# Kernel optimization log

Hardware: AMD Instinct MI355X
Metric: run time of the kernel (lower is better)

## Reference

```python
import jax, jax.numpy as jnp
import numpy as np

B, C, CI, H, W = 8, 256, 128, 64, 64
EPS = 1e-5


def conv1x1(x, w, b):
    # x: [B,C,H,W], w: [O,C], b: [O] -> [B,O,H,W]
    return jnp.einsum('bchw,oc->bohw', x, w) + b[None, :, None, None]


def maxpool2(x):
    # 2x2 max pool, stride 2 (NCHW)
    b, c, h, w = x.shape
    return x.reshape(b, c, h // 2, 2, w // 2, 2).max(axis=(3, 5))


def setup_inputs() -> dict:
    key = jax.random.key(0)
    ks = jax.random.split(key, 14)
    s_in = 1.0 / np.sqrt(C)
    s_ci = 1.0 / np.sqrt(CI)
    return {
        'x': jax.random.normal(ks[0], (B, C, H, W), jnp.float32),
        'w_theta': jax.random.normal(ks[1], (CI, C), jnp.float32) * s_in,
        'b_theta': jax.random.normal(ks[2], (CI,), jnp.float32) * 0.01,
        'w_phi': jax.random.normal(ks[3], (CI, C), jnp.float32) * s_in,
        'b_phi': jax.random.normal(ks[4], (CI,), jnp.float32) * 0.01,
        'w_g': jax.random.normal(ks[5], (CI, C), jnp.float32) * s_in,
        'b_g': jax.random.normal(ks[6], (CI,), jnp.float32) * 0.01,
        'w_w': jax.random.normal(ks[7], (C, CI), jnp.float32) * s_ci,
        'b_w': jax.random.normal(ks[8], (C,), jnp.float32) * 0.01,
        'bn_gamma': jax.random.normal(ks[9], (C,), jnp.float32) * 0.1,
        'bn_beta': jax.random.normal(ks[10], (C,), jnp.float32) * 0.1,
        'bn_mean': jax.random.normal(ks[11], (C,), jnp.float32) * 0.1,
        'bn_var': jax.random.uniform(ks[12], (C,), jnp.float32) + 0.5,
    }


def reference(x, w_theta, b_theta, w_phi, b_phi, w_g, b_g,
              w_w, b_w, bn_gamma, bn_beta, bn_mean, bn_var):
    b = x.shape[0]
    theta_x = conv1x1(x, w_theta, b_theta).reshape(b, CI, -1)            # [B,Ci,N]
    phi_x = maxpool2(conv1x1(x, w_phi, b_phi)).reshape(b, CI, -1)        # [B,Ci,M]
    g_x = maxpool2(conv1x1(x, w_g, b_g)).reshape(b, CI, -1)              # [B,Ci,M]
    m = phi_x.shape[-1]
    # unnormalized attention: f = theta^T phi / M  -> [B,N,M]
    f = jnp.einsum('bcn,bcm->bnm', theta_x, phi_x) / m
    y = jnp.einsum('bnm,bcm->bcn', f, g_x).reshape(b, CI, H, W)          # [B,Ci,H,W]
    w_y = conv1x1(y, w_w, b_w)                                           # [B,C,H,W]
    inv = jax.lax.rsqrt(bn_var + EPS)
    bn = (w_y - bn_mean[None, :, None, None]) * (bn_gamma * inv)[None, :, None, None] \
         + bn_beta[None, :, None, None]
    return bn + x
```

## Files before the change

kernel.cpp:

```cpp
#include <hip/hip_runtime.h>


typedef __attribute__((ext_vector_type(8))) short bf16x8;
typedef __attribute__((ext_vector_type(4))) float f32x4;
typedef unsigned short u16;
typedef unsigned int u32;

constexpr int Cc = 256, NnC = 4096;
constexpr float kEps = 1e-5f;

__device__ __forceinline__ u16 f2b(float f) {
  u32 u = __float_as_uint(f);
  return (u16)((u + 0x7fffu + ((u >> 16) & 1u)) >> 16);
}
__device__ __forceinline__ float b2f(u16 h) {
  return __uint_as_float(((u32)h) << 16);
}
__device__ __forceinline__ u32 pack2(float a, float b) {
  return (u32)f2b(a) | ((u32)f2b(b) << 16);
}
__device__ __forceinline__ void gl16(const void* g, void* l) {
  __builtin_amdgcn_global_load_lds(
      (const __attribute__((address_space(1))) void*)g,
      (__attribute__((address_space(3))) void*)l, 16, 0, 0);
}

__global__ __launch_bounds__(256) void prepw_kernel(
    const float* __restrict__ wp, const float* __restrict__ wg,
    u16* __restrict__ Wfg) {
  const int idx = blockIdx.x * 256 + threadIdx.x;
  const int r = idx >> 8, c = idx & 255;
  Wfg[idx] = f2b(r < 128 ? wp[r * 256 + c] : wg[(r - 128) * 256 + c]);
}

__global__ __launch_bounds__(256) void prepx_kernel(const float* __restrict__ x,
                                                    u16* __restrict__ xT) {
  __shared__ float sm[64][65];
  const int b = blockIdx.z, c0 = blockIdx.y * 64, n0 = blockIdx.x * 64;
  const int tid = threadIdx.x;
  {
    const int n = tid & 63, cg = tid >> 6;
#pragma unroll
    for (int i = 0; i < 16; ++i) {
      const int c = cg * 16 + i;
      sm[c][n] = x[((size_t)(b * Cc + c0 + c)) * NnC + n0 + n];
    }
  }
  __syncthreads();
  {
    const int n = tid >> 2, q = tid & 3;
    u16 v[16];
#pragma unroll
    for (int j = 0; j < 16; ++j) v[j] = f2b(sm[q * 16 + j][n]);
    uint4 o0, o1;
    o0.x = v[0] | ((u32)v[1] << 16);
    o0.y = v[2] | ((u32)v[3] << 16);
    o0.z = v[4] | ((u32)v[5] << 16);
    o0.w = v[6] | ((u32)v[7] << 16);
    o1.x = v[8] | ((u32)v[9] << 16);
    o1.y = v[10] | ((u32)v[11] << 16);
    o1.z = v[12] | ((u32)v[13] << 16);
    o1.w = v[14] | ((u32)v[15] << 16);
    uint4* dst = (uint4*)(xT + ((size_t)(b * NnC + n0 + n)) * Cc + c0 + q * 16);
    dst[0] = o0;
    dst[1] = o1;
  }
}

__global__ __launch_bounds__(256) void convfg_kernel(
    const u16* __restrict__ xT, const u16* __restrict__ Wfg,
    const float* __restrict__ b_phi, const float* __restrict__ b_g,
    u16* __restrict__ phiT, u16* __restrict__ gT) {
  __shared__ u16 sm[2][2][8192];
  const int mt = blockIdx.x, nt = blockIdx.y, b = blockIdx.z;
  const int n0 = nt * 128;
  const int tid = threadIdx.x;
  const int w = tid >> 6, lane = tid & 63;
  const int r16 = lane & 15, kg = lane >> 4;
  const int oh = (w & 1) * 64, nh = (w >> 1) * 64;

  auto stage = [&](int buf, int k0) {
#pragma unroll
    for (int i = 0; i < 4; ++i) {
      const int lin = i * 4096 + tid * 16;
      const int row = lin >> 7, byte = lin & 127;
      gl16((const char*)Wfg + (size_t)(mt * 128 + row) * 512 + k0 * 2 +
               (byte ^ ((row & 7) << 4)),
           (char*)&sm[buf][0][0] + lin);
    }
#pragma unroll
    for (int i = 0; i < 4; ++i) {
      const int lin = i * 4096 + tid * 16;
      const int row = lin >> 7, byte = lin & 127;
      gl16((const char*)xT + ((size_t)(b * NnC + n0 + row) * Cc + k0) * 2 +
               (byte ^ ((row & 7) << 4)),
           (char*)&sm[buf][1][0] + lin);
    }
  };

  f32x4 acc[4][4];
#pragma unroll
  for (int i = 0; i < 4; ++i)
#pragma unroll
    for (int j = 0; j < 4; ++j) acc[i][j] = (f32x4)0.f;

  stage(0, 0);
  __syncthreads();
  for (int kt = 0; kt < 4; ++kt) {
    if (kt < 3) stage((kt + 1) & 1, (kt + 1) * 64);
    const char* A = (const char*)&sm[kt & 1][0][0];
    const char* Bm = (const char*)&sm[kt & 1][1][0];
#pragma unroll
    for (int ks = 0; ks < 2; ++ks) {
      bf16x8 af[4], bfr[4];
#pragma unroll
      for (int f = 0; f < 4; ++f) {
        const int o = oh + f * 16 + r16;
        af[f] = *(const bf16x8*)(A + ((o * 128 + ks * 64 + kg * 16) ^
                                      ((o & 7) << 4)));
        const int n = nh + f * 16 + r16;
        bfr[f] = *(const bf16x8*)(Bm + ((n * 128 + ks * 64 + kg * 16) ^
                                        ((n & 7) << 4)));
      }
#pragma unroll
      for (int fo = 0; fo < 4; ++fo)
#pragma unroll
        for (int fn = 0; fn < 4; ++fn)
          acc[fo][fn] = __builtin_amdgcn_mfma_f32_16x16x32_bf16(
              af[fo], bfr[fn], acc[fo][fn], 0, 0, 0);
    }
    __syncthreads();
  }

  const float* bias = (mt == 0) ? b_phi : b_g;
  u16* ldst = (u16*)&sm[0][0][0];
#pragma unroll
  for (int fo = 0; fo < 4; ++fo) {
    const int obase = oh + fo * 16 + kg * 4;
    const float b0 = bias[obase], b1 = bias[obase + 1], b2 = bias[obase + 2],
                b3 = bias[obase + 3];
#pragma unroll
    for (int fn = 0; fn < 4; ++fn) {
      const int n = nh + fn * 16 + r16;
      const f32x4 v = acc[fo][fn];
      uint2 p;
      p.x = pack2(v.x + b0, v.y + b1);
      p.y = pack2(v.z + b2, v.w + b3);
      *(uint2*)((char*)ldst + ((n * 256 + obase * 2) ^ ((n & 7) << 4))) = p;
    }
  }
  __syncthreads();

  u16* dst = (mt == 0) ? phiT : gT;
  const int ci = tid >> 1, half = tid & 1;
#pragma unroll
  for (int i = 0; i < 16; ++i) {
    const int mw = half * 16 + i;
    const int n00 = 2 * mw;
    float v0 = b2f(*(const u16*)((const char*)ldst +
                                 ((n00 * 256 + ci * 2) ^ ((n00 & 7) << 4))));
    float v1 = b2f(*(const u16*)((const char*)ldst +
                                 (((n00 + 1) * 256 + ci * 2) ^ (((n00 + 1) & 7) << 4))));
    float v2 = b2f(*(const u16*)((const char*)ldst +
                                 (((n00 + 64) * 256 + ci * 2) ^ (((n00 + 64) & 7) << 4))));
    float v3 = b2f(*(const u16*)((const char*)ldst +
                                 (((n00 + 65) * 256 + ci * 2) ^ (((n00 + 65) & 7) << 4))));
    const float mx = fmaxf(fmaxf(v0, v1), fmaxf(v2, v3));
    dst[((size_t)(b * 128 + ci)) * 1024 + nt * 32 + mw] = f2b(mx);
  }
}

__global__ __launch_bounds__(256) void g2_kernel(const u16* __restrict__ phiT,
                                                 const u16* __restrict__ gT,
                                                 float* __restrict__ A_g2) {
  __shared__ u16 sm[2][12288];
  const int ch0 = blockIdx.x * 64, b = blockIdx.y;
  const int tid = threadIdx.x;
  const int w = tid >> 6, lane = tid & 63;
  const int r16 = lane & 15, kg = lane >> 4;
  const int cih = (w & 1) * 64, cch = (w >> 1) * 32;

  auto stage = [&](int buf, int m0) {
#pragma unroll
    for (int i = 0; i < 4; ++i) {
      const int lin = i * 4096 + tid * 16;
      const int row = lin >> 7, byte = lin & 127;
      gl16((const char*)gT + ((size_t)(b * 128 + row) * 1024 + m0) * 2 +
               (byte ^ ((row & 7) << 4)),
           (char*)&sm[buf][0] + lin);
    }
#pragma unroll
    for (int i = 0; i < 2; ++i) {
      const int lin = i * 4096 + tid * 16;
      const int row = lin >> 7, byte = lin & 127;
      gl16((const char*)phiT + ((size_t)(b * 128 + ch0 + row) * 1024 + m0) * 2 +
               (byte ^ ((row & 7) << 4)),
           (char*)&sm[buf][8192] + lin);
    }
  };

  f32x4 acc[4][2];
#pragma unroll
  for (int i = 0; i < 4; ++i)
#pragma unroll
    for (int j = 0; j < 2; ++j) acc[i][j] = (f32x4)0.f;

  stage(0, 0);
  __syncthreads();
  for (int kt = 0; kt < 16; ++kt) {
    if (kt < 15) stage((kt + 1) & 1, (kt + 1) * 64);
    const char* A = (const char*)&sm[kt & 1][0];
    const char* Bp = A + 16384;
#pragma unroll
    for (int ks = 0; ks < 2; ++ks) {
      bf16x8 af[4], bfr[2];
#pragma unroll
      for (int f = 0; f < 4; ++f) {
        const int o = cih + f * 16 + r16;
        af[f] = *(const bf16x8*)(A + ((o * 128 + ks * 64 + kg * 16) ^
                                      ((o & 7) << 4)));
      }
#pragma unroll
      for (int f = 0; f < 2; ++f) {
        const int lc = cch + f * 16 + r16;
        bfr[f] = *(const bf16x8*)(Bp + ((lc * 128 + ks * 64 + kg * 16) ^
                                        ((lc & 7) << 4)));
      }
#pragma unroll
      for (int fo = 0; fo < 4; ++fo)
#pragma unroll
        for (int fn = 0; fn < 2; ++fn)
          acc[fo][fn] = __builtin_amdgcn_mfma_f32_16x16x32_bf16(
              af[fo], bfr[fn], acc[fo][fn], 0, 0, 0);
    }
    __syncthreads();
  }

  constexpr float scl = 1.f / 1024.f;
#pragma unroll
  for (int fo = 0; fo < 4; ++fo) {
#pragma unroll
    for (int r = 0; r < 4; ++r) {
      const int ci = cih + fo * 16 + kg * 4 + r;
#pragma unroll
      for (int fn = 0; fn < 2; ++fn) {
        const int c = ch0 + cch + fn * 16 + r16;
        A_g2[(size_t)b * 16384 + ci * 128 + c] = acc[fo][fn][r] * scl;
      }
    }
  }
}

__global__ __launch_bounds__(256) void t1_kernel(const float* __restrict__ A_g2,
                                                 const float* __restrict__ w_theta,
                                                 float* __restrict__ T1) {
  __shared__ float As[16][128];
  __shared__ float Ws[128][17];
  const int tile = blockIdx.x, b = blockIdx.y;
  const int ci0 = (tile >> 4) * 16, j0 = (tile & 15) * 16;
  const int t = threadIdx.x;
#pragma unroll
  for (int i = 0; i < 8; ++i) {
    const int idx = t + i * 256;
    As[idx >> 7][idx & 127] =
        A_g2[(size_t)b * 16384 + (ci0 + (idx >> 7)) * 128 + (idx & 127)];
    Ws[idx >> 4][idx & 15] = w_theta[(idx >> 4) * 256 + j0 + (idx & 15)];
  }
  __syncthreads();
  const int tci = t >> 4, tj = t & 15;
  float s = 0.f;
#pragma unroll 8
  for (int c = 0; c < 128; ++c) s = fmaf(As[tci][c], Ws[c][tj], s);
  T1[(size_t)b * 32768 + (ci0 + tci) * 256 + j0 + tj] = s;
}

__global__ __launch_bounds__(256) void wbig_kernel(
    const float* __restrict__ T1, const float* __restrict__ A_g2,
    const float* __restrict__ w_w, const float* __restrict__ b_theta,
    const float* __restrict__ b_w, u16* __restrict__ Wbig,
    float* __restrict__ beff) {
  __shared__ float Ws2[16][128];
  __shared__ float T1s[128][17];
  __shared__ float v1[128];
  const int tile = blockIdx.x, b = blockIdx.y;
  const int t = threadIdx.x;
  if (tile < 256) {
    const int o0 = (tile >> 4) * 16, j0 = (tile & 15) * 16;
#pragma unroll
    for (int i = 0; i < 8; ++i) {
      const int idx = t + i * 256;
      Ws2[idx >> 7][idx & 127] = w_w[(o0 + (idx >> 7)) * 128 + (idx & 127)];
      T1s[idx >> 4][idx & 15] =
          T1[(size_t)b * 32768 + (idx >> 4) * 256 + j0 + (idx & 15)];
    }
    __syncthreads();
    const int to = t >> 4, tj = t & 15;
    float s = 0.f;
#pragma unroll 8
    for (int c = 0; c < 128; ++c) s = fmaf(Ws2[to][c], T1s[c][tj], s);
    Wbig[(size_t)b * 65536 + (o0 + to) * 256 + j0 + tj] = f2b(s);
  } else {
    if (t < 128) {
      float s = 0.f;
      for (int c = 0; c < 128; ++c)
        s = fmaf(A_g2[(size_t)b * 16384 + t * 128 + c], b_theta[c], s);
      v1[t] = s;
    }
    __syncthreads();
    float s2 = b_w[t];
    for (int ci = 0; ci < 128; ++ci) s2 = fmaf(w_w[t * 128 + ci], v1[ci], s2);
    beff[b * 256 + t] = s2;
  }
}

__global__ __launch_bounds__(256) void final_kernel(
    const u16* __restrict__ xT, const u16* __restrict__ Wbig,
    const float* __restrict__ beff, const float* __restrict__ gamma,
    const float* __restrict__ beta, const float* __restrict__ mean,
    const float* __restrict__ var, const float* __restrict__ x,
    float* __restrict__ out) {
  __shared__ u16 sm[2][2][8192];
  __shared__ float scs[128], offs[128];
  const int mt = blockIdx.x, nt = blockIdx.y, b = blockIdx.z;
  const int n0 = nt * 128;
  const int tid = threadIdx.x;
  const int w = tid >> 6, lane = tid & 63;
  const int r16 = lane & 15, kg = lane >> 4;
  const int oh = (w & 1) * 64, nh = (w >> 1) * 64;

  if (tid < 128) {
    const int o = mt * 128 + tid;
    const float sc = gamma[o] * rsqrtf(var[o] + kEps);
    scs[tid] = sc;
    offs[tid] = beta[o] + (beff[b * 256 + o] - mean[o]) * sc;
  }

  auto stage = [&](int buf, int k0) {
#pragma unroll
    for (int i = 0; i < 4; ++i) {
      const int lin = i * 4096 + tid * 16;
      const int row = lin >> 7, byte = lin & 127;
      gl16((const char*)Wbig + (size_t)b * 131072 +
               (size_t)(mt * 128 + row) * 512 + k0 * 2 +
               (byte ^ ((row & 7) << 4)),
           (char*)&sm[buf][0][0] + lin);
    }
#pragma unroll
    for (int i = 0; i < 4; ++i) {
      const int lin = i * 4096 + tid * 16;
      const int row = lin >> 7, byte = lin & 127;
      gl16((const char*)xT + ((size_t)(b * NnC + n0 + row) * Cc + k0) * 2 +
               (byte ^ ((row & 7) << 4)),
           (char*)&sm[buf][1][0] + lin);
    }
  };

  f32x4 acc[4][4];
#pragma unroll
  for (int i = 0; i < 4; ++i)
#pragma unroll
    for (int j = 0; j < 4; ++j) acc[i][j] = (f32x4)0.f;

  stage(0, 0);
  __syncthreads();
  for (int kt = 0; kt < 4; ++kt) {
    if (kt < 3) stage((kt + 1) & 1, (kt + 1) * 64);
    const char* A = (const char*)&sm[kt & 1][0][0];
    const char* Bm = (const char*)&sm[kt & 1][1][0];
#pragma unroll
    for (int ks = 0; ks < 2; ++ks) {
      bf16x8 af[4], bfr[4];
#pragma unroll
      for (int f = 0; f < 4; ++f) {
        const int o = oh + f * 16 + r16;
        af[f] = *(const bf16x8*)(A + ((o * 128 + ks * 64 + kg * 16) ^
                                      ((o & 7) << 4)));
        const int n = nh + f * 16 + r16;
        bfr[f] = *(const bf16x8*)(Bm + ((n * 128 + ks * 64 + kg * 16) ^
                                        ((n & 7) << 4)));
      }
#pragma unroll
      for (int fo = 0; fo < 4; ++fo)
#pragma unroll
        for (int fn = 0; fn < 4; ++fn)
          acc[fo][fn] = __builtin_amdgcn_mfma_f32_16x16x32_bf16(
              af[fo], bfr[fn], acc[fo][fn], 0, 0, 0);
    }
    __syncthreads();
  }

  const size_t xb = ((size_t)b * Cc + mt * 128) * NnC;
#pragma unroll
  for (int fo = 0; fo < 4; ++fo) {
#pragma unroll
    for (int r = 0; r < 4; ++r) {
      const int ol = oh + fo * 16 + kg * 4 + r;
      const float sc = scs[ol], of = offs[ol];
      const size_t rowoff = xb + (size_t)ol * NnC + n0;
#pragma unroll
      for (int fn = 0; fn < 4; ++fn) {
        const int n = nh + fn * 16 + r16;
        out[rowoff + n] = fmaf(acc[fo][fn][r], sc, of) + x[rowoff + n];
      }
    }
  }
}

extern "C" void kernel_launch(void* const* d_in, const int* in_sizes, int n_in,
                              void* d_out, int out_size, void* d_ws,
                              size_t ws_size, hipStream_t stream) {
  const float* x = (const float*)d_in[0];
  const float* w_theta = (const float*)d_in[1];
  const float* b_theta = (const float*)d_in[2];
  const float* w_phi = (const float*)d_in[3];
  const float* b_phi = (const float*)d_in[4];
  const float* w_g = (const float*)d_in[5];
  const float* b_g = (const float*)d_in[6];
  const float* w_w = (const float*)d_in[7];
  const float* b_w = (const float*)d_in[8];
  const float* bn_gamma = (const float*)d_in[9];
  const float* bn_beta = (const float*)d_in[10];
  const float* bn_mean = (const float*)d_in[11];
  const float* bn_var = (const float*)d_in[12];
  float* out = (float*)d_out;

  char* ws = (char*)d_ws;
  u16* xT = (u16*)ws;
  u16* Wfg = (u16*)(ws + 16777216);
  u16* phiT = (u16*)(ws + 16908288);
  u16* gT = (u16*)(ws + 19005440);
  float* A_g2 = (float*)(ws + 21102592);
  float* T1 = (float*)(ws + 21626880);
  u16* Wbig = (u16*)(ws + 22675456);
  float* beff = (float*)(ws + 23724032);
  if (ws_size < 23732224ull) return;

  prepw_kernel<<<dim3(256), dim3(256), 0, stream>>>(w_phi, w_g, Wfg);
  prepx_kernel<<<dim3(64, 4, 8), dim3(256), 0, stream>>>(x, xT);
  convfg_kernel<<<dim3(2, 32, 8), dim3(256), 0, stream>>>(
      xT, Wfg, b_phi, b_g, phiT, gT);
  g2_kernel<<<dim3(2, 8), dim3(256), 0, stream>>>(phiT, gT, A_g2);
  t1_kernel<<<dim3(128, 8), dim3(256), 0, stream>>>(A_g2, w_theta, T1);
  wbig_kernel<<<dim3(257, 8), dim3(256), 0, stream>>>(T1, A_g2, w_w, b_theta,
                                                      b_w, Wbig, beff);
  final_kernel<<<dim3(2, 32, 8), dim3(256), 0, stream>>>(
      xT, Wbig, beff, bn_gamma, bn_beta, bn_mean, bn_var, x, out);
}
```

Before: 157.6 us.

## Fuse weight/x bf16 conversion and transpose into phi/g convolution kernel

Merges the weight conversion, x transpose/convert, and phi/g conv+maxpool kernels into one 512-thread kernel that reads fp32 x and weights directly. Each block now computes both phi and g outputs (256 output channels) for its 128-pixel tile, so x is loaded once instead of twice, and it still writes xT for the final kernel. This removes two launches and the xT round-trip read, but the grid shrinks to 256 blocks with large LDS use and loses the async double-buffered global-to-LDS loads, so loads are no longer overlapped with MFMA work.

Result: no change. 160.0 us (+1.5%).

```diff
diff --git a/kernel.cpp b/kernel.cpp
--- a/kernel.cpp
+++ b/kernel.cpp
@@ -25,78 +25,21 @@
       (__attribute__((address_space(3))) void*)l, 16, 0, 0);
 }
 
-__global__ __launch_bounds__(256) void prepw_kernel(
-    const float* __restrict__ wp, const float* __restrict__ wg,
-    u16* __restrict__ Wfg) {
-  const int idx = blockIdx.x * 256 + threadIdx.x;
-  const int r = idx >> 8, c = idx & 255;
-  Wfg[idx] = f2b(r < 128 ? wp[r * 256 + c] : wg[(r - 128) * 256 + c]);
-}
-
-__global__ __launch_bounds__(256) void prepx_kernel(const float* __restrict__ x,
-                                                    u16* __restrict__ xT) {
-  __shared__ float sm[64][65];
-  const int b = blockIdx.z, c0 = blockIdx.y * 64, n0 = blockIdx.x * 64;
-  const int tid = threadIdx.x;
-  {
-    const int n = tid & 63, cg = tid >> 6;
-#pragma unroll
-    for (int i = 0; i < 16; ++i) {
-      const int c = cg * 16 + i;
-      sm[c][n] = x[((size_t)(b * Cc + c0 + c)) * NnC + n0 + n];
-    }
-  }
-  __syncthreads();
-  {
-    const int n = tid >> 2, q = tid & 3;
-    u16 v[16];
-#pragma unroll
-    for (int j = 0; j < 16; ++j) v[j] = f2b(sm[q * 16 + j][n]);
-    uint4 o0, o1;
-    o0.x = v[0] | ((u32)v[1] << 16);
-    o0.y = v[2] | ((u32)v[3] << 16);
-    o0.z = v[4] | ((u32)v[5] << 16);
-    o0.w = v[6] | ((u32)v[7] << 16);
-    o1.x = v[8] | ((u32)v[9] << 16);
-    o1.y = v[10] | ((u32)v[11] << 16);
-    o1.z = v[12] | ((u32)v[13] << 16);
-    o1.w = v[14] | ((u32)v[15] << 16);
-    uint4* dst = (uint4*)(xT + ((size_t)(b * NnC + n0 + n)) * Cc + c0 + q * 16);
-    dst[0] = o0;
-    dst[1] = o1;
-  }
-}
-
-__global__ __launch_bounds__(256) void convfg_kernel(
-    const u16* __restrict__ xT, const u16* __restrict__ Wfg,
-    const float* __restrict__ b_phi, const float* __restrict__ b_g,
+__global__ __launch_bounds__(512) void convfg2_kernel(
+    const float* __restrict__ x, const float* __restrict__ w_phi,
+    const float* __restrict__ w_g, const float* __restrict__ b_phi,
+    const float* __restrict__ b_g, u16* __restrict__ xT,
     u16* __restrict__ phiT, u16* __restrict__ gT) {
-  __shared__ u16 sm[2][2][8192];
-  const int mt = blockIdx.x, nt = blockIdx.y, b = blockIdx.z;
+  __shared__ __align__(16) char pool[83968];
+  float* xf = (float*)pool;
+  char* Asm = pool + 34816;
+  char* Bsm = pool + 67584;
+  const int nt = blockIdx.x, b = blockIdx.y;
   const int n0 = nt * 128;
-  const int tid = threadIdx.x;
-  const int w = tid >> 6, lane = tid & 63;
+  const int t = threadIdx.x;
+  const int w = t >> 6, lane = t & 63;
   const int r16 = lane & 15, kg = lane >> 4;
-  const int oh = (w & 1) * 64, nh = (w >> 1) * 64;
-
-  auto stage = [&](int buf, int k0) {
-#pragma unroll
-    for (int i = 0; i < 4; ++i) {
-      const int lin = i * 4096 + tid * 16;
-      const int row = lin >> 7, byte = lin & 127;
-      gl16((const char*)Wfg + (size_t)(mt * 128 + row) * 512 + k0 * 2 +
-               (byte ^ ((row & 7) << 4)),
-           (char*)&sm[buf][0][0] + lin);
-    }
-#pragma unroll
-    for (int i = 0; i < 4; ++i) {
-      const int lin = i * 4096 + tid * 16;
-      const int row = lin >> 7, byte = lin & 127;
-      gl16((const char*)xT + ((size_t)(b * NnC + n0 + row) * Cc + k0) * 2 +
-               (byte ^ ((row & 7) << 4)),
-           (char*)&sm[buf][1][0] + lin);
-    }
-  };
+  const int oh = (w & 3) * 64, nh = (w >> 2) * 64;
 
   f32x4 acc[4][4];
 #pragma unroll
@@ -104,23 +47,64 @@
 #pragma unroll
     for (int j = 0; j < 4; ++j) acc[i][j] = (f32x4)0.f;
 
-  stage(0, 0);
-  __syncthreads();
   for (int kt = 0; kt < 4; ++kt) {
-    if (kt < 3) stage((kt + 1) & 1, (kt + 1) * 64);
-    const char* A = (const char*)&sm[kt & 1][0][0];
-    const char* Bm = (const char*)&sm[kt & 1][1][0];
+    const int c0 = kt * 64;
+    {
+      const int o = t >> 1, cc0 = (t & 1) * 32;
+      const float* wsrc = (o < 128) ? (w_phi + (size_t)o * 256 + c0 + cc0)
+                                    : (w_g + (size_t)(o - 128) * 256 + c0 + cc0);
+#pragma unroll
+      for (int j = 0; j < 4; ++j) {
+        const float4 v0 = *(const float4*)(wsrc + j * 8);
+        const float4 v1 = *(const float4*)(wsrc + j * 8 + 4);
+        uint4 p;
+        p.x = pack2(v0.x, v0.y);
+        p.y = pack2(v0.z, v0.w);
+        p.z = pack2(v1.x, v1.y);
+        p.w = pack2(v1.z, v1.w);
+        *(uint4*)(Asm + ((o * 128 + (cc0 + j * 8) * 2) ^ ((o & 7) << 4))) = p;
+      }
+    }
+    {
+      const int n4 = (t & 31) * 4;
+#pragma unroll
+      for (int i = 0; i < 4; ++i) {
+        const int cc = (t >> 5) + i * 16;
+        const float4 v =
+            *(const float4*)(x + (size_t)(b * Cc + c0 + cc) * NnC + n0 + n4);
+        *(float4*)(xf + cc * 136 + n4) = v;
+      }
+    }
+    __syncthreads();
+    {
+      const int c8 = (t & 7) * 8;
+#pragma unroll
+      for (int i = 0; i < 2; ++i) {
+        const int n = (t >> 3) + i * 64;
+        float f[8];
+#pragma unroll
+        for (int cc = 0; cc < 8; ++cc) f[cc] = xf[(c8 + cc) * 136 + n];
+        uint4 p;
+        p.x = pack2(f[0], f[1]);
+        p.y = pack2(f[2], f[3]);
+        p.z = pack2(f[4], f[5]);
+        p.w = pack2(f[6], f[7]);
+        *(uint4*)(Bsm + ((n * 128 + c8 * 2) ^ ((n & 7) << 4))) = p;
+        *(uint4*)(xT + (size_t)(b * NnC + n0 + n) * Cc + c0 + c8) = p;
+      }
+    }
+    __syncthreads();
 #pragma unroll
     for (int ks = 0; ks < 2; ++ks) {
       bf16x8 af[4], bfr[4];
 #pragma unroll
       for (int f = 0; f < 4; ++f) {
         const int o = oh + f * 16 + r16;
-        af[f] = *(const bf16x8*)(A + ((o * 128 + ks * 64 + kg * 16) ^
-                                      ((o & 7) << 4)));
+        af[f] = *(const bf16x8*)(Asm + ((o * 128 + ks * 64 + kg * 16) ^
+                                        ((o & 7) << 4)));
         const int n = nh + f * 16 + r16;
-        bfr[f] = *(const bf16x8*)(Bm + ((n * 128 + ks * 64 + kg * 16) ^
-                                        ((n & 7) << 4)));
+        bfr[f] = *(const bf16x8*)(Bsm + ((n * 128 + ks * 64 + kg * 16) ^
+                                         ((n & 7) << 4)));
       }
 #pragma unroll
       for (int fo = 0; fo < 4; ++fo)
@@ -132,13 +116,12 @@
     __syncthreads();
   }
 
-  const float* bias = (mt == 0) ? b_phi : b_g;
-  u16* ldst = (u16*)&sm[0][0][0];
+  u16* tile = (u16*)pool;
 #pragma unroll
   for (int fo = 0; fo < 4; ++fo) {
     const int obase = oh + fo * 16 + kg * 4;
-    const float b0 = bias[obase], b1 = bias[obase + 1], b2 = bias[obase + 2],
-                b3 = bias[obase + 3];
+    const float* bias = (obase < 128) ? (b_phi + obase) : (b_g + obase - 128);
+    const float b0 = bias[0], b1 = bias[1], b2 = bias[2], b3 = bias[3];
 #pragma unroll
     for (int fn = 0; fn < 4; ++fn) {
       const int n = nh + fn * 16 + r16;
@@ -146,27 +129,34 @@
       uint2 p;
       p.x = pack2(v.x + b0, v.y + b1);
       p.y = pack2(v.z + b2, v.w + b3);
-      *(uint2*)((char*)ldst + ((n * 256 + obase * 2) ^ ((n & 7) << 4))) = p;
+      *(uint2*)((char*)tile + ((n * 512 + obase * 2) ^ ((n & 7) << 4))) = p;
     }
   }
   __syncthreads();
-
-  u16* dst = (mt == 0) ? phiT : gT;
-  const int ci = tid >> 1, half = tid & 1;
-#pragma unroll
-  for (int i = 0; i < 16; ++i) {
-    const int mw = half * 16 + i;
-    const int n00 = 2 * mw;
-    float v0 = b2f(*(const u16*)((const char*)ldst +
-                                 ((n00 * 256 + ci * 2) ^ ((n00 & 7) << 4))));
-    float v1 = b2f(*(const u16*)((const char*)ldst +
-                                 (((n00 + 1) * 256 + ci * 2) ^ (((n00 + 1) & 7) << 4))));
-    float v2 = b2f(*(const u16*)((const char*)ldst +
-                                 (((n00 + 64) * 256 + ci * 2) ^ (((n00 + 64) & 7) << 4))));
-    float v3 = b2f(*(const u16*)((const char*)ldst +
-                                 (((n00 + 65) * 256 + ci * 2) ^ (((n00 + 65) & 7) << 4))));
-    const float mx = fmaxf(fmaxf(v0, v1), fmaxf(v2, v3));
-    dst[((size_t)(b * 128 + ci)) * 1024 + nt * 32 + mw] = f2b(mx);
+  {
+    const int tsel = t >> 8;
+    const int r = t & 255;
+    const int ci = r >> 1, half = r & 1;
+    const int o2 = (tsel * 128 + ci) * 2;
+    u16* dst = tsel ? gT : phiT;
+#pragma unroll
+    for (int i = 0; i < 16; ++i) {
+      const int mw = half * 16 + i;
+      const int n00 = 2 * mw;
+      const float v0 = b2f(*(const u16*)((const char*)tile +
+                                         ((n00 * 512 + o2) ^ ((n00 & 7) << 4))));
+      const float v1 = b2f(*(const u16*)((const char*)tile +
+                                         (((n00 + 1) * 512 + o2) ^
+                                          (((n00 + 1) & 7) << 4))));
+      const float v2 = b2f(*(const u16*)((const char*)tile +
+                                         (((n00 + 64) * 512 + o2) ^
+                                          (((n00 + 64) & 7) << 4))));
+      const float v3 = b2f(*(const u16*)((const char*)tile +
+                                         (((n00 + 65) * 512 + o2) ^
+                                          (((n00 + 65) & 7) << 4))));
+      const float mx = fmaxf(fmaxf(v0, v1), fmaxf(v2, v3));
+      dst[(size_t)(b * 128 + ci) * 1024 + nt * 32 + mw] = f2b(mx);
+    }
   }
 }
 
@@ -426,19 +416,16 @@
 
   char* ws = (char*)d_ws;
   u16* xT = (u16*)ws;
-  u16* Wfg = (u16*)(ws + 16777216);
-  u16* phiT = (u16*)(ws + 16908288);
-  u16* gT = (u16*)(ws + 19005440);
-  float* A_g2 = (float*)(ws + 21102592);
-  float* T1 = (float*)(ws + 21626880);
-  u16* Wbig = (u16*)(ws + 22675456);
-  float* beff = (float*)(ws + 23724032);
-  if (ws_size < 23732224ull) return;
-
-  prepw_kernel<<<dim3(256), dim3(256), 0, stream>>>(w_phi, w_g, Wfg);
-  prepx_kernel<<<dim3(64, 4, 8), dim3(256), 0, stream>>>(x, xT);
-  convfg_kernel<<<dim3(2, 32, 8), dim3(256), 0, stream>>>(
-      xT, Wfg, b_phi, b_g, phiT, gT);
+  u16* phiT = (u16*)(ws + 16777216);
+  u16* gT = (u16*)(ws + 18874368);
+  float* A_g2 = (float*)(ws + 20971520);
+  float* T1 = (float*)(ws + 21495808);
+  u16* Wbig = (u16*)(ws + 22544384);
+  float* beff = (float*)(ws + 23592960);
+  if (ws_size < 23601152ull) return;
+
+  convfg2_kernel<<<dim3(32, 8), dim3(512), 0, stream>>>(
+      x, w_phi, w_g, b_phi, b_g, xT, phiT, gT);
   g2_kernel<<<dim3(2, 8), dim3(256), 0, stream>>>(phiT, gT, A_g2);
   t1_kernel<<<dim3(128, 8), dim3(256), 0, stream>>>(A_g2, w_theta, T1);
   wbig_kernel<<<dim3(257, 8), dim3(256), 0, stream>>>(T1, A_g2, w_w, b_theta,
```

## Fuse g2, t1 and wbig chain into one per-batch MFMA kernel; enlarge final tiles

Applied to the files above, without the earlier changes.

Replaces the three small kernels (g2, t1, wbig) with a single chain_kernel that runs one 512-thread block per batch. It keeps the intermediates (A_g2 and T1) in LDS as bf16 and computes the T1 and Wbig products with MFMA instead of scalar FMA loops. This removes two launches and the global round-trips of the intermediates, but runs only 8 blocks and rounds the intermediates to bf16. final_kernel moves to 512 threads with 256-column N tiles, halving its grid.

Measured after the change: 164.6 us. 4.4% more time.

```diff
diff --git a/kernel.cpp b/kernel.cpp
--- a/kernel.cpp
+++ b/kernel.cpp
@@ -170,188 +170,275 @@
   }
 }
 
-__global__ __launch_bounds__(256) void g2_kernel(const u16* __restrict__ phiT,
-                                                 const u16* __restrict__ gT,
-                                                 float* __restrict__ A_g2) {
-  __shared__ u16 sm[2][12288];
-  const int ch0 = blockIdx.x * 64, b = blockIdx.y;
-  const int tid = threadIdx.x;
-  const int w = tid >> 6, lane = tid & 63;
+__global__ __launch_bounds__(512) void chain_kernel(
+    const u16* __restrict__ phiT, const u16* __restrict__ gT,
+    const float* __restrict__ w_theta, const float* __restrict__ w_w,
+    const float* __restrict__ b_theta, const float* __restrict__ b_w,
+    u16* __restrict__ Wbig, float* __restrict__ beff) {
+  __shared__ __align__(16) char pool[163840];
+  char* abp = pool + 65536;
+  char* t1b = pool + 98304;
+  const int b = blockIdx.x;
+  const int t = threadIdx.x;
+  const int w = t >> 6, lane = t & 63;
   const int r16 = lane & 15, kg = lane >> 4;
-  const int cih = (w & 1) * 64, cch = (w >> 1) * 32;
-
-  auto stage = [&](int buf, int m0) {
-#pragma unroll
-    for (int i = 0; i < 4; ++i) {
-      const int lin = i * 4096 + tid * 16;
-      const int row = lin >> 7, byte = lin & 127;
-      gl16((const char*)gT + ((size_t)(b * 128 + row) * 1024 + m0) * 2 +
-               (byte ^ ((row & 7) << 4)),
-           (char*)&sm[buf][0] + lin);
-    }
-#pragma unroll
-    for (int i = 0; i < 2; ++i) {
-      const int lin = i * 4096 + tid * 16;
-      const int row = lin >> 7, byte = lin & 127;
-      gl16((const char*)phiT + ((size_t)(b * 128 + ch0 + row) * 1024 + m0) * 2 +
-               (byte ^ ((row & 7) << 4)),
-           (char*)&sm[buf][8192] + lin);
-    }
-  };
-
-  f32x4 acc[4][2];
-#pragma unroll
-  for (int i = 0; i < 4; ++i)
-#pragma unroll
-    for (int j = 0; j < 2; ++j) acc[i][j] = (f32x4)0.f;
-
-  stage(0, 0);
+  const int cih = (w & 1) * 64;
+
+  {
+    const int cch = (w >> 1) * 32;
+    auto stage1 = [&](int buf, int m0) {
+      char* base = pool + buf * 32768;
+#pragma unroll
+      for (int i = 0; i < 2; ++i) {
+        const int lin = i * 8192 + t * 16;
+        const int row = lin >> 7, byte = lin & 127;
+        gl16((const char*)gT + ((size_t)(b * 128 + row) * 1024 + m0) * 2 +
+                 (byte ^ ((row & 7) << 4)),
+             base + lin);
+      }
+#pragma unroll
+      for (int i = 0; i < 2; ++i) {
+        const int lin = i * 8192 + t * 16;
+        const int row = lin >> 7, byte = lin & 127;
+        gl16((const char*)phiT + ((size_t)(b * 128 + row) * 1024 + m0) * 2 +
+                 (byte ^ ((row & 7) << 4)),
+             base + 16384 + lin);
+      }
+    };
+    f32x4 acc1[4][2];
+#pragma unroll
+    for (int i = 0; i < 4; ++i)
+#pragma unroll
+      for (int j = 0; j < 2; ++j) acc1[i][j] = (f32x4)0.f;
+    stage1(0, 0);
+    __syncthreads();
+    for (int kt = 0; kt < 16; ++kt) {
+      if (kt < 15) stage1((kt + 1) & 1, (kt + 1) * 64);
+      const char* A = pool + (kt & 1) * 32768;
+      const char* Bp = A + 16384;
+#pragma unroll
+      for (int ks = 0; ks < 2; ++ks) {
+        bf16x8 af[4], bfr[2];
+#pragma unroll
+        for (int f = 0; f < 4; ++f) {
+          const int o = cih + f * 16 + r16;
+          af[f] = *(const bf16x8*)(A + ((o * 128 + ks * 64 + kg * 16) ^
+                                        ((o & 7) << 4)));
+        }
+#pragma unroll
+        for (int f = 0; f < 2; ++f) {
+          const int lc = cch + f * 16 + r16;
+          bfr[f] = *(const bf16x8*)(Bp + ((lc * 128 + ks * 64 + kg * 16) ^
+                                          ((lc & 7) << 4)));
+        }
+#pragma unroll
+        for (int fo = 0; fo < 4; ++fo)
+#pragma unroll
+          for (int fn = 0; fn < 2; ++fn)
+            acc1[fo][fn] = __builtin_amdgcn_mfma_f32_16x16x32_bf16(
+                af[fo], bfr[fn], acc1[fo][fn], 0, 0, 0);
+      }
+      __syncthreads();
+    }
+    constexpr float scl = 1.f / 1024.f;
+#pragma unroll
+    for (int fo = 0; fo < 4; ++fo)
+#pragma unroll
+      for (int fn = 0; fn < 2; ++fn)
+#pragma unroll
+        for (int r = 0; r < 4; ++r) {
+          const int ci = cih + fo * 16 + kg * 4 + r;
+          const int c = cch + fn * 16 + r16;
+          *(u16*)(abp + ((ci * 256 + c * 2) ^ ((ci & 7) << 4))) =
+              f2b(acc1[fo][fn][r] * scl);
+        }
+    __syncthreads();
+  }
+
+  {
+    float* wf = (float*)pool;
+    char* wtb = pool + 36864;
+    const int jq = w >> 1;
+    for (int j0 = 0; j0 < 256; j0 += 64) {
+      {
+        const int c2 = t >> 2, q = t & 3;
+#pragma unroll
+        for (int i = 0; i < 4; ++i) {
+          const float4 v =
+              *(const float4*)(w_theta + (size_t)c2 * 256 + j0 + q * 16 + i * 4);
+          *(float4*)(wf + c2 * 68 + q * 16 + i * 4) = v;
+        }
+      }
+      __syncthreads();
+      {
+        const int jl = t & 63, cg = t >> 6;
+        float f[16];
+#pragma unroll
+        for (int k = 0; k < 16; ++k) f[k] = wf[(cg * 16 + k) * 68 + jl];
+        uint4 p0, p1;
+        p0.x = pack2(f[0], f[1]);
+        p0.y = pack2(f[2], f[3]);
+        p0.z = pack2(f[4], f[5]);
+        p0.w = pack2(f[6], f[7]);
+        p1.x = pack2(f[8], f[9]);
+        p1.y = pack2(f[10], f[11]);
+        p1.z = pack2(f[12], f[13]);
+        p1.w = pack2(f[14], f[15]);
+        *(uint4*)(wtb + ((jl * 256 + cg * 32) ^ ((jl & 7) << 4))) = p0;
+        *(uint4*)(wtb + ((jl * 256 + cg * 32 + 16) ^ ((jl & 7) << 4))) = p1;
+      }
+      __syncthreads();
+      f32x4 acc2[4];
+#pragma unroll
+      for (int i = 0; i < 4; ++i) acc2[i] = (f32x4)0.f;
+#pragma unroll
+      for (int ks = 0; ks < 4; ++ks) {
+        bf16x8 af[4];
+#pragma unroll
+        for (int fo = 0; fo < 4; ++fo) {
+          const int ci = cih + fo * 16 + r16;
+          af[fo] = *(const bf16x8*)(abp + ((ci * 256 + ks * 64 + kg * 16) ^
+                                           ((ci & 7) << 4)));
+        }
+        const int jl = jq * 16 + r16;
+        const bf16x8 bfr = *(const bf16x8*)(wtb + ((jl * 256 + ks * 64 + kg * 16) ^
+                                                   ((jl & 7) << 4)));
+#pragma unroll
+        for (int fo = 0; fo < 4; ++fo)
+          acc2[fo] = __builtin_amdgcn_mfma_f32_16x16x32_bf16(af[fo], bfr,
+                                                             acc2[fo], 0, 0, 0);
+      }
+      const int jg = j0 + jq * 16 + r16;
+#pragma unroll
+      for (int fo = 0; fo < 4; ++fo) {
+        const int cib = cih + fo * 16 + kg * 4;
+        uint2 p;
+        p.x = pack2(acc2[fo][0], acc2[fo][1]);
+        p.y = pack2(acc2[fo][2], acc2[fo][3]);
+        *(uint2*)(t1b + ((jg * 256 + cib * 2) ^ ((jg & 7) << 4))) = p;
+      }
+      __syncthreads();
+    }
+  }
+
+  {
+    {
+      const int o = t >> 1, half = (t & 1) * 64;
+#pragma unroll
+      for (int j = 0; j < 8; ++j) {
+        const float4 v0 = *(const float4*)(w_w + (size_t)o * 128 + half + j * 8);
+        const float4 v1 =
+            *(const float4*)(w_w + (size_t)o * 128 + half + j * 8 + 4);
+        uint4 p;
+        p.x = pack2(v0.x, v0.y);
+        p.y = pack2(v0.z, v0.w);
+        p.z = pack2(v1.x, v1.y);
+        p.w = pack2(v1.z, v1.w);
+        *(uint4*)(pool + ((o * 256 + (half + j * 8) * 2) ^ ((o & 7) << 4))) = p;
+      }
+    }
+    __syncthreads();
+    const int oq = (w & 3) * 64, jh = (w >> 2) * 128;
+#pragma unroll
+    for (int jp = 0; jp < 2; ++jp) {
+      f32x4 acc3[4][4];
+#pragma unroll
+      for (int i = 0; i < 4; ++i)
+#pragma unroll
+        for (int j = 0; j < 4; ++j) acc3[i][j] = (f32x4)0.f;
+#pragma unroll
+      for (int ks = 0; ks < 4; ++ks) {
+        bf16x8 af[4], bfr[4];
+#pragma unroll
+        for (int fo = 0; fo < 4; ++fo) {
+          const int o = oq + fo * 16 + r16;
+          af[fo] = *(const bf16x8*)(pool + ((o * 256 + ks * 64 + kg * 16) ^
+                                            ((o & 7) << 4)));
+        }
+#pragma unroll
+        for (int fn = 0; fn < 4; ++fn) {
+          const int j = jh + jp * 64 + fn * 16 + r16;
+          bfr[fn] = *(const bf16x8*)(t1b + ((j * 256 + ks * 64 + kg * 16) ^
+                                            ((j & 7) << 4)));
+        }
+#pragma unroll
+        for (int fo = 0; fo < 4; ++fo)
+#pragma unroll
+          for (int fn = 0; fn < 4; ++fn)
+            acc3[fo][fn] = __builtin_amdgcn_mfma_f32_16x16x32_bf16(
+                af[fo], bfr[fn], acc3[fo][fn], 0, 0, 0);
+      }
+#pragma unroll
+      for (int fo = 0; fo < 4; ++fo)
+#pragma unroll
+        for (int fn = 0; fn < 4; ++fn)
+#pragma unroll
+          for (int r = 0; r < 4; ++r) {
+            const int o = oq + fo * 16 + kg * 4 + r;
+            const int j = jh + jp * 64 + fn * 16 + r16;
+            Wbig[(size_t)b * 65536 + o * 256 + j] = f2b(acc3[fo][fn][r]);
+          }
+    }
+  }
+
+  float vreg = 0.f;
+  if (t < 128) {
+    for (int c = 0; c < 128; ++c)
+      vreg += b2f(*(const u16*)(abp + ((t * 256 + c * 2) ^ ((t & 7) << 4)))) *
+              b_theta[c];
+  }
   __syncthreads();
-  for (int kt = 0; kt < 16; ++kt) {
-    if (kt < 15) stage((kt + 1) & 1, (kt + 1) * 64);
-    const char* A = (const char*)&sm[kt & 1][0];
-    const char* Bp = A + 16384;
-#pragma unroll
-    for (int ks = 0; ks < 2; ++ks) {
-      bf16x8 af[4], bfr[2];
-#pragma unroll
-      for (int f = 0; f < 4; ++f) {
-        const int o = cih + f * 16 + r16;
-        af[f] = *(const bf16x8*)(A + ((o * 128 + ks * 64 + kg * 16) ^
-                                      ((o & 7) << 4)));
-      }
-#pragma unroll
-      for (int f = 0; f < 2; ++f) {
-        const int lc = cch + f * 16 + r16;
-        bfr[f] = *(const bf16x8*)(Bp + ((lc * 128 + ks * 64 + kg * 16) ^
-                                        ((lc & 7) << 4)));
-      }
-#pragma unroll
-      for (int fo = 0; fo < 4; ++fo)
-#pragma unroll
-        for (int fn = 0; fn < 2; ++fn)
-          acc[fo][fn] = __builtin_amdgcn_mfma_f32_16x16x32_bf16(
-              af[fo], bfr[fn], acc[fo][fn], 0, 0, 0);
-    }
-    __syncthreads();
-  }
-
-  constexpr float scl = 1.f / 1024.f;
-#pragma unroll
-  for (int fo = 0; fo < 4; ++fo) {
-#pragma unroll
-    for (int r = 0; r < 4; ++r) {
-      const int ci = cih + fo * 16 + kg * 4 + r;
-#pragma unroll
-      for (int fn = 0; fn < 2; ++fn) {
-        const int c = ch0 + cch + fn * 16 + r16;
-        A_g2[(size_t)b * 16384 + ci * 128 + c] = acc[fo][fn][r] * scl;
-      }
-    }
-  }
-}
-
-__global__ __launch_bounds__(256) void t1_kernel(const float* __restrict__ A_g2,
-                                                 const float* __restrict__ w_theta,
-                                                 float* __restrict__ T1) {
-  __shared__ float As[16][128];
-  __shared__ float Ws[128][17];
-  const int tile = blockIdx.x, b = blockIdx.y;
-  const int ci0 = (tile >> 4) * 16, j0 = (tile & 15) * 16;
-  const int t = threadIdx.x;
-#pragma unroll
-  for (int i = 0; i < 8; ++i) {
-    const int idx = t + i * 256;
-    As[idx >> 7][idx & 127] =
-        A_g2[(size_t)b * 16384 + (ci0 + (idx >> 7)) * 128 + (idx & 127)];
-    Ws[idx >> 4][idx & 15] = w_theta[(idx >> 4) * 256 + j0 + (idx & 15)];
-  }
+  if (t < 128) ((float*)abp)[t] = vreg;
   __syncthreads();
-  const int tci = t >> 4, tj = t & 15;
-  float s = 0.f;
-#pragma unroll 8
-  for (int c = 0; c < 128; ++c) s = fmaf(As[tci][c], Ws[c][tj], s);
-  T1[(size_t)b * 32768 + (ci0 + tci) * 256 + j0 + tj] = s;
-}
-
-__global__ __launch_bounds__(256) void wbig_kernel(
-    const float* __restrict__ T1, const float* __restrict__ A_g2,
-    const float* __restrict__ w_w, const float* __restrict__ b_theta,
-    const float* __restrict__ b_w, u16* __restrict__ Wbig,
-    float* __restrict__ beff) {
-  __shared__ float Ws2[16][128];
-  __shared__ float T1s[128][17];
-  __shared__ float v1[128];
-  const int tile = blockIdx.x, b = blockIdx.y;
-  const int t = threadIdx.x;
-  if (tile < 256) {
-    const int o0 = (tile >> 4) * 16, j0 = (tile & 15) * 16;
-#pragma unroll
-    for (int i = 0; i < 8; ++i) {
-      const int idx = t + i * 256;
-      Ws2[idx >> 7][idx & 127] = w_w[(o0 + (idx >> 7)) * 128 + (idx & 127)];
-      T1s[idx >> 4][idx & 15] =
-          T1[(size_t)b * 32768 + (idx >> 4) * 256 + j0 + (idx & 15)];
-    }
-    __syncthreads();
-    const int to = t >> 4, tj = t & 15;
-    float s = 0.f;
-#pragma unroll 8
-    for (int c = 0; c < 128; ++c) s = fmaf(Ws2[to][c], T1s[c][tj], s);
-    Wbig[(size_t)b * 65536 + (o0 + to) * 256 + j0 + tj] = f2b(s);
-  } else {
-    if (t < 128) {
-      float s = 0.f;
-      for (int c = 0; c < 128; ++c)
-        s = fmaf(A_g2[(size_t)b * 16384 + t * 128 + c], b_theta[c], s);
-      v1[t] = s;
-    }
-    __syncthreads();
-    float s2 = b_w[t];
-    for (int ci = 0; ci < 128; ++ci) s2 = fmaf(w_w[t * 128 + ci], v1[ci], s2);
-    beff[b * 256 + t] = s2;
-  }
-}
-
-__global__ __launch_bounds__(256) void final_kernel(
+  if (t < 256) {
+    float s = b_w[t];
+    const float* v1 = (const float*)abp;
+    for (int ci = 0; ci < 128; ++ci)
+      s += b2f(*(const u16*)(pool + ((t * 256 + ci * 2) ^ ((t & 7) << 4)))) *
+           v1[ci];
+    beff[b * 256 + t] = s;
+  }
+}
+
+__global__ __launch_bounds__(512) void final_kernel(
     const u16* __restrict__ xT, const u16* __restrict__ Wbig,
     const float* __restrict__ beff, const float* __restrict__ gamma,
     const float* __restrict__ beta, const float* __restrict__ mean,
     const float* __restrict__ var, const float* __restrict__ x,
     float* __restrict__ out) {
-  __shared__ u16 sm[2][2][8192];
+  __shared__ __align__(16) char sm[2][49152];
   __shared__ float scs[128], offs[128];
   const int mt = blockIdx.x, nt = blockIdx.y, b = blockIdx.z;
-  const int n0 = nt * 128;
-  const int tid = threadIdx.x;
-  const int w = tid >> 6, lane = tid & 63;
+  const int n0 = nt * 256;
+  const int t = threadIdx.x;
+  const int w = t >> 6, lane = t & 63;
   const int r16 = lane & 15, kg = lane >> 4;
   const int oh = (w & 1) * 64, nh = (w >> 1) * 64;
 
-  if (tid < 128) {
-    const int o = mt * 128 + tid;
+  if (t < 128) {
+    const int o = mt * 128 + t;
     const float sc = gamma[o] * rsqrtf(var[o] + kEps);
-    scs[tid] = sc;
-    offs[tid] = beta[o] + (beff[b * 256 + o] - mean[o]) * sc;
+    scs[t] = sc;
+    offs[t] = beta[o] + (beff[b * 256 + o] - mean[o]) * sc;
   }
 
   auto stage = [&](int buf, int k0) {
 #pragma unroll
-    for (int i = 0; i < 4; ++i) {
-      const int lin = i * 4096 + tid * 16;
+    for (int i = 0; i < 2; ++i) {
+      const int lin = i * 8192 + t * 16;
       const int row = lin >> 7, byte = lin & 127;
       gl16((const char*)Wbig + (size_t)b * 131072 +
                (size_t)(mt * 128 + row) * 512 + k0 * 2 +
                (byte ^ ((row & 7) << 4)),
-           (char*)&sm[buf][0][0] + lin);
+           (char*)&sm[buf][0] + lin);
     }
 #pragma unroll
     for (int i = 0; i < 4; ++i) {
-      const int lin = i * 4096 + tid * 16;
+      const int lin = i * 8192 + t * 16;
       const int row = lin >> 7, byte = lin & 127;
       gl16((const char*)xT + ((size_t)(b * NnC + n0 + row) * Cc + k0) * 2 +
                (byte ^ ((row & 7) << 4)),
-           (char*)&sm[buf][1][0] + lin);
+           (char*)&sm[buf][16384] + lin);
     }
   };
 
@@ -365,8 +452,8 @@
   __syncthreads();
   for (int kt = 0; kt < 4; ++kt) {
     if (kt < 3) stage((kt + 1) & 1, (kt + 1) * 64);
-    const char* A = (const char*)&sm[kt & 1][0][0];
-    const char* Bm = (const char*)&sm[kt & 1][1][0];
+    const char* A = (const char*)&sm[kt & 1][0];
+    const char* Bm = A + 16384;
 #pragma unroll
     for (int ks = 0; ks < 2; ++ks) {
       bf16x8 af[4], bfr[4];
@@ -429,20 +516,16 @@
   u16* Wfg = (u16*)(ws + 16777216);
   u16* phiT = (u16*)(ws + 16908288);
   u16* gT = (u16*)(ws + 19005440);
-  float* A_g2 = (float*)(ws + 21102592);
-  float* T1 = (float*)(ws + 21626880);
-  u16* Wbig = (u16*)(ws + 22675456);
-  float* beff = (float*)(ws + 23724032);
-  if (ws_size < 23732224ull) return;
+  u16* Wbig = (u16*)(ws + 21102592);
+  float* beff = (float*)(ws + 22151168);
+  if (ws_size < 22159360ull) return;
 
   prepw_kernel<<<dim3(256), dim3(256), 0, stream>>>(w_phi, w_g, Wfg);
   prepx_kernel<<<dim3(64, 4, 8), dim3(256), 0, stream>>>(x, xT);
   convfg_kernel<<<dim3(2, 32, 8), dim3(256), 0, stream>>>(
       xT, Wfg, b_phi, b_g, phiT, gT);
-  g2_kernel<<<dim3(2, 8), dim3(256), 0, stream>>>(phiT, gT, A_g2);
-  t1_kernel<<<dim3(128, 8), dim3(256), 0, stream>>>(A_g2, w_theta, T1);
-  wbig_kernel<<<dim3(257, 8), dim3(256), 0, stream>>>(T1, A_g2, w_w, b_theta,
-                                                      b_w, Wbig, beff);
-  final_kernel<<<dim3(2, 32, 8), dim3(256), 0, stream>>>(
+  chain_kernel<<<dim3(8), dim3(512), 0, stream>>>(phiT, gT, w_theta, w_w,
+                                                  b_theta, b_w, Wbig, beff);
+  final_kernel<<<dim3(2, 16, 8), dim3(512), 0, stream>>>(
       xT, Wbig, beff, bn_gamma, bn_beta, bn_mean, bn_var, x, out);
 }
```
